# Optimization experiments

Hardware: AMD Instinct MI355X
Metric: run time of the kernel (lower is better)

Reference implementation:

```python
import jax, jax.numpy as jnp
import numpy as np

B = 32768   # batch
D = 64      # latent_dimension_half
H = 256     # inner_dimension
T = D * (D + 1) // 2  # 2080 triangular outputs


def setup_inputs() -> dict:
    key = jax.random.key(0)
    ks = jax.random.split(key, 7)
    s = 0.05
    return {
        "x": jax.random.normal(ks[0], (B, D), dtype=jnp.float32),
        "W1": jax.random.normal(ks[1], (D, H), dtype=jnp.float32) * s,
        "b1": jax.random.normal(ks[2], (H,), dtype=jnp.float32) * s,
        "W2": jax.random.normal(ks[3], (H, H), dtype=jnp.float32) * s,
        "b2": jax.random.normal(ks[4], (H,), dtype=jnp.float32) * s,
        "W3": jax.random.normal(ks[5], (H, T), dtype=jnp.float32) * s,
        "b3": jax.random.normal(ks[6], (T,), dtype=jnp.float32) * s,
    }


def reference(x, W1, b1, W2, b2, W3, b3):
    d = x.shape[-1]  # latent_dimension_half
    h = jnp.tanh(x @ W1 + b1)
    h = jnp.tanh(h @ W2 + b2)
    t = jnp.tanh(h @ W3 + b3)  # [B, d*(d+1)/2]
    # scatter: first d entries -> diagonal (diagflat), rest -> strict upper
    # triangle in row-major order (matches torch boolean-mask assignment)
    di = np.arange(d)
    iu, ju = np.triu_indices(d, k=1)
    rows = np.concatenate([di, iu])
    cols = np.concatenate([di, ju])
    u = jnp.zeros((x.shape[0], d, d), dtype=t.dtype).at[:, rows, cols].set(t)
    # y[b] = u[b].T @ u[b]
    return jnp.einsum('bki,bkj->bij', u, u)
```

## Files before the change

kernel.cpp:

```cpp
#include <hip/hip_runtime.h>


typedef __bf16 bf16_t;
typedef bf16_t bf16x8 __attribute__((ext_vector_type(8)));
typedef float  f32x4  __attribute__((ext_vector_type(4)));

#define MFMA16(a, b, c) __builtin_amdgcn_mfma_f32_16x16x32_bf16((a), (b), (c), 0, 0, 0)

constexpr int SLOT  = 4608;
constexpr int ARENA = 73728;
constexpr int H2OFF = 147456;
constexpr int CTRL  = 155648;

__device__ __forceinline__ float fast_tanh(float x) {
  float cx = fminf(fmaxf(x, -30.0f), 30.0f);
  float t  = __expf(2.0f * cx);
  return (t - 1.0f) * __builtin_amdgcn_rcpf(t + 1.0f);
}

__device__ __forceinline__ bf16x8 zsel(bf16x8 f, bool keep) {
  union { bf16x8 v; unsigned int u[4]; } x;
  x.v = f;
  unsigned m = keep ? 0xFFFFFFFFu : 0u;
#pragma unroll
  for (int p = 0; p < 4; ++p) x.u[p] &= m;
  return x.v;
}

__device__ __forceinline__ void decode_p(int p, int& j, int& k) {
  int cc = p >> 3, e = p & 7;
  int b = 0;
  while (b < 7 && cc >= 4 * (b + 1) * (b + 2)) ++b;
  int rl  = b + 1;
  int rem = cc - 4 * b * (b + 1);
  j = 8 * b + rem / rl;
  k = (rem % rl) * 8 + e;
}

__device__ __forceinline__ void lds_arrive(unsigned* p, int lane) {
  asm volatile("s_waitcnt lgkmcnt(0)" ::: "memory");
  if (lane == 0) atomicAdd(p, 1u);
}
__device__ __forceinline__ void lds_wait(volatile unsigned* p, unsigned tgt) {
  while (*p < tgt) __builtin_amdgcn_s_sleep(2);
  asm volatile("" ::: "memory");
  __builtin_amdgcn_sched_barrier(0);
}

__global__ void prep_kernel(const float* __restrict__ W1, const float* __restrict__ W2,
                            const float* __restrict__ W3, const float* __restrict__ b3,
                            char* __restrict__ wsb) {
  int tid = blockIdx.x * 512 + threadIdx.x;
  bf16_t* ws = (bf16_t*)wsb;
  if (tid < 16384) {
    int n = tid >> 6, k = tid & 63;
    ws[tid] = (bf16_t)W1[k * 256 + n];
  } else if (tid < 81920) {
    int m = tid - 16384;
    int n = m >> 8, k = m & 255;
    ws[tid] = (bf16_t)W2[k * 256 + n];
  } else if (tid < 671744) {
    int m = tid - 81920;
    int t  = m >> 12;
    int r  = m & 4095;
    int kk = r >> 9;
    int g  = (r >> 7) & 3;
    int c  = (r >> 3) & 15;
    int e  = r & 7;
    int p  = t * 16 + c;
    int k  = kk * 32 + g * 8 + e;
    int j, kd;
    decode_p(p, j, kd);
    float v = 0.f;
    if (kd <= j) {
      int n_ref = (kd == j) ? j : (64 + kd * 63 - (kd * (kd - 1)) / 2 + j - kd - 1);
      v = W3[k * 2080 + n_ref];
    }
    ws[tid] = (bf16_t)v;
  } else if (tid < 674048) {
    int p = tid - 671744;
    int j, kd;
    decode_p(p, j, kd);
    float v = 0.f;
    if (kd <= j) {
      int n_ref = (kd == j) ? j : (64 + kd * 63 - (kd * (kd - 1)) / 2 + j - kd - 1);
      v = b3[n_ref];
    }
    ((float*)(wsb + 1343488))[p] = v;
  }
}

__device__ __forceinline__ void gram_store(char* slot, int sw, float* yb,
                                           int g, int c, int lane) {
  bf16x8 f0, f1, f2, f3, f2b, f3b;
#pragma unroll
  for (int ti = 0; ti < 4; ++ti) {
    int j = ti * 16 + c;
    int Q = j >> 3, s = j & 7;
    int ro = 16 * (4 * Q * (Q + 1) + s * (Q + 1));
    bf16x8 fa = *(const bf16x8*)(slot + ((ro + g * 16) ^ sw));
    if (ti == 0) f0 = zsel(fa, g * 8 <= j);
    if (ti == 1) f1 = zsel(fa, g * 8 <= j);
    if (ti == 2) f2 = fa;
    if (ti == 3) f3 = fa;
    if (ti >= 2) {
      bf16x8 fb = *(const bf16x8*)(slot + ((ro + 64 + g * 16) ^ sw));
      fb = zsel(fb, 32 + g * 8 <= j);
      if (ti == 2) f2b = fb;
      else         f3b = fb;
    }
  }

  bf16x8 fA[4] = {f0, f1, f2, f3};
  f32x4 acc[4][4];
#pragma unroll
  for (int ti = 0; ti < 4; ++ti)
#pragma unroll
    for (int tj = 0; tj < 4; ++tj) {
      f32x4 z = {0.f, 0.f, 0.f, 0.f};
      acc[ti][tj] = MFMA16(fA[ti], fA[tj], z);
    }
  acc[2][2] = MFMA16(f2b, f2b, acc[2][2]);
  acc[2][3] = MFMA16(f2b, f3b, acc[2][3]);
  acc[3][2] = MFMA16(f3b, f2b, acc[3][2]);
  acc[3][3] = MFMA16(f3b, f3b, acc[3][3]);

#pragma unroll
  for (int ti = 0; ti < 4; ++ti) {
#pragma unroll
    for (int tj = 0; tj < 4; ++tj)
#pragma unroll
      for (int r = 0; r < 4; ++r)
        *(float*)(slot + (g * 4 + r) * 256 + (tj * 16 + c) * 4) = acc[ti][tj][r];
#pragma unroll
    for (int ii = 0; ii < 4; ++ii) {
      f32x4 v = *(const f32x4*)(slot + ii * 1024 + lane * 16);
      __builtin_nontemporal_store(v, (f32x4*)(yb + ti * 1024 + ii * 256 + lane * 4));
    }
  }
}

__global__ void __launch_bounds__(768, 3)
hm_kernel(const float* __restrict__ x, const float* __restrict__ b1,
          const float* __restrict__ b2, const char* __restrict__ wsb,
          float* __restrict__ out) {
  extern __shared__ char smem[];
  const int tid  = threadIdx.x;
  const int w    = tid >> 6;
  const int lane = tid & 63;
  const int g    = lane >> 4;
  const int c    = lane & 15;
  const int blk  = blockIdx.x;

  const bf16_t* W1t = (const bf16_t*)wsb;
  const bf16_t* W2t = W1t + 16384;
  const bf16_t* W3q = W1t + 81920;
  const float*  b3p = (const float*)(wsb + 1343488);
  char* h2s = smem + H2OFF;
  unsigned* ctrl = (unsigned*)(smem + CTRL);

  if (tid < 40) ctrl[tid] = 0;
  __syncthreads();

  if (w < 8) {
    float bias1[2], bias2[2];
#pragma unroll
    for (int ni = 0; ni < 2; ++ni) {
      int n = (w * 2 + ni) * 16 + c;
      bias1[ni] = b1[n];
      bias2[ni] = b2[n];
    }

#pragma unroll 1
    for (int r = 0; r < 8; ++r) {
      char* cur = smem + (r & 1) * ARENA;
      char* xs  = cur;
      char* h1s = cur + 4096;

      if (r >= 2) lds_wait(&ctrl[32 + (r - 2)], 4);

      if (tid < 256) {
        f32x4 v = *(const f32x4*)(x + ((size_t)blk * 128 + r * 16) * 64 + tid * 4);
        int row = tid >> 4, col = (tid & 15) * 4;
        union { bf16_t b[4]; unsigned long long u; } pk;
        pk.b[0] = (bf16_t)v[0]; pk.b[1] = (bf16_t)v[1];
        pk.b[2] = (bf16_t)v[2]; pk.b[3] = (bf16_t)v[3];
        *(unsigned long long*)(xs + ((row * 128 + col * 2) ^ ((row & 7) << 4))) = pk.u;
      }
      lds_arrive(&ctrl[r * 3 + 0], lane); lds_wait(&ctrl[r * 3 + 0], 8);

      {
        bf16x8 a0 = *(const bf16x8*)(xs + ((c * 128 + g * 16) ^ ((c & 7) << 4)));
        bf16x8 a1 = *(const bf16x8*)(xs + ((c * 128 + 64 + g * 16) ^ ((c & 7) << 4)));
#pragma unroll
        for (int ni = 0; ni < 2; ++ni) {
          int n = (w * 2 + ni) * 16 + c;
          bf16x8 bw0 = *(const bf16x8*)(W1t + n * 64 + g * 8);
          bf16x8 bw1 = *(const bf16x8*)(W1t + n * 64 + 32 + g * 8);
          f32x4 acc = {0.f, 0.f, 0.f, 0.f};
          acc = MFMA16(a0, bw0, acc);
          acc = MFMA16(a1, bw1, acc);
#pragma unroll
          for (int rr = 0; rr < 4; ++rr) {
            int row = g * 4 + rr;
            float v = fast_tanh(acc[rr] + bias1[ni]);
            *(bf16_t*)(h1s + ((row * 512 + n * 2) ^ ((row & 7) << 4))) = (bf16_t)v;
          }
        }
      }
      lds_arrive(&ctrl[r * 3 + 1], lane); lds_wait(&ctrl[r * 3 + 1], 8);

#pragma unroll
      for (int ni = 0; ni < 2; ++ni) {
        int n = (w * 2 + ni) * 16 + c;
        f32x4 acc0 = {0.f, 0.f, 0.f, 0.f}, acc1 = {0.f, 0.f, 0.f, 0.f};
#pragma unroll
        for (int kk = 0; kk < 8; kk += 2) {
          bf16x8 a0 = *(const bf16x8*)(h1s + ((c * 512 + kk * 64 + g * 16) ^ ((c & 7) << 4)));
          bf16x8 a1 = *(const bf16x8*)(h1s + ((c * 512 + (kk + 1) * 64 + g * 16) ^ ((c & 7) << 4)));
          bf16x8 bw0 = *(const bf16x8*)(W2t + n * 256 + kk * 32 + g * 8);
          bf16x8 bw1 = *(const bf16x8*)(W2t + n * 256 + (kk + 1) * 32 + g * 8);
          acc0 = MFMA16(a0, bw0, acc0);
          acc1 = MFMA16(a1, bw1, acc1);
        }
        f32x4 acc = acc0 + acc1;
#pragma unroll
        for (int rr = 0; rr < 4; ++rr) {
          int row = g * 4 + rr;
          float v = fast_tanh(acc[rr] + bias2[ni]);
          *(bf16_t*)(h2s + ((row * 512 + n * 2) ^ ((row & 7) << 4))) = (bf16_t)v;
        }
      }
      lds_arrive(&ctrl[r * 3 + 2], lane); lds_wait(&ctrl[r * 3 + 2], 8);

      {
        bf16x8 a0 = *(const bf16x8*)(h2s + ((c * 512 + 0 * 64 + g * 16) ^ ((c & 7) << 4)));
        bf16x8 a1 = *(const bf16x8*)(h2s + ((c * 512 + 1 * 64 + g * 16) ^ ((c & 7) << 4)));
        bf16x8 a2 = *(const bf16x8*)(h2s + ((c * 512 + 2 * 64 + g * 16) ^ ((c & 7) << 4)));
        bf16x8 a3 = *(const bf16x8*)(h2s + ((c * 512 + 3 * 64 + g * 16) ^ ((c & 7) << 4)));
        bf16x8 a4 = *(const bf16x8*)(h2s + ((c * 512 + 4 * 64 + g * 16) ^ ((c & 7) << 4)));
        bf16x8 a5 = *(const bf16x8*)(h2s + ((c * 512 + 5 * 64 + g * 16) ^ ((c & 7) << 4)));
        bf16x8 a6 = *(const bf16x8*)(h2s + ((c * 512 + 6 * 64 + g * 16) ^ ((c & 7) << 4)));
        bf16x8 a7 = *(const bf16x8*)(h2s + ((c * 512 + 7 * 64 + g * 16) ^ ((c & 7) << 4)));

        char* tw = cur + (g * 4) * SLOT;
        const int swz = (g & 7) << 4;

        bf16x8 A0, A1, A2, A3, A4, A5, A6, A7; float Ab;
        bf16x8 B0, B1, B2, B3, B4, B5, B6, B7; float Bb;

#define ISSUE_T(S, TI)                                                              \
  do {                                                                              \
    int t_ = w + (TI) * 8;                                                          \
    const bf16_t* np_ = W3q + t_ * 4096 + lane * 8;                                 \
    asm volatile("global_load_dwordx4 %0, %1, off" : "=v"(S##0) : "v"(np_));            \
    asm volatile("global_load_dwordx4 %0, %1, off" : "=v"(S##1) : "v"(np_ + 512));      \
    asm volatile("global_load_dwordx4 %0, %1, off" : "=v"(S##2) : "v"(np_ + 1024));     \
    asm volatile("global_load_dwordx4 %0, %1, off" : "=v"(S##3) : "v"(np_ + 1536));     \
    asm volatile("global_load_dwordx4 %0, %1, off" : "=v"(S##4) : "v"(np_ + 2048));     \
    asm volatile("global_load_dwordx4 %0, %1, off" : "=v"(S##5) : "v"(np_ + 2560));     \
    asm volatile("global_load_dwordx4 %0, %1, off" : "=v"(S##6) : "v"(np_ + 3072));     \
    asm volatile("global_load_dwordx4 %0, %1, off" : "=v"(S##7) : "v"(np_ + 3584));     \
    asm volatile("global_load_dword %0, %1, off"   : "=v"(S##b) : "v"(b3p + t_ * 16 + c)); \
  } while (0)

#define WAIT_N(N)                                          \
  do {                                                     \
    asm volatile("s_waitcnt vmcnt(" #N ")" ::: "memory");  \
    __builtin_amdgcn_sched_barrier(0);                     \
  } while (0)

#define COMP_T(S, TI)                                                    \
  do {                                                                   \
    f32x4 acc0 = {S##b, S##b, S##b, S##b};                               \
    f32x4 acc1 = {0.f, 0.f, 0.f, 0.f};                                   \
    acc0 = MFMA16(a0, S##0, acc0); acc1 = MFMA16(a1, S##1, acc1);        \
    acc0 = MFMA16(a2, S##2, acc0); acc1 = MFMA16(a3, S##3, acc1);        \
    acc0 = MFMA16(a4, S##4, acc0); acc1 = MFMA16(a5, S##5, acc1);        \
    acc0 = MFMA16(a6, S##6, acc0); acc1 = MFMA16(a7, S##7, acc1);        \
    f32x4 accs = acc0 + acc1;                                            \
    int p_ = (w + (TI) * 8) * 16 + c;                                    \
    _Pragma("unroll")                                                    \
    for (int r_ = 0; r_ < 4; ++r_) {                                     \
      float v_ = fast_tanh(accs[r_]);                                    \
      *(bf16_t*)(tw + r_ * SLOT + ((p_ * 2) ^ swz)) = (bf16_t)v_;        \
    }                                                                    \
  } while (0)

        ISSUE_T(A, 0);
#pragma unroll 1
        for (int pr = 0; pr < 8; ++pr) {
          ISSUE_T(B, 2 * pr + 1);
          WAIT_N(9);
          COMP_T(A, 2 * pr);
          ISSUE_T(A, 2 * pr + 2);
          WAIT_N(9);
          COMP_T(B, 2 * pr + 1);
        }
        ISSUE_T(B, 17);
        WAIT_N(9);
        COMP_T(A, 16);
        WAIT_N(0);
        COMP_T(B, 17);

#undef ISSUE_T
#undef WAIT_N
#undef COMP_T
      }
      lds_arrive(&ctrl[24 + r], lane);
    }
  } else {
    int ww = w - 8;
#pragma unroll 1
    for (int r = 0; r < 8; ++r) {
      lds_wait(&ctrl[24 + r], 8);
      char* arena = smem + (r & 1) * ARENA;
#pragma unroll 1
      for (int bi = 0; bi < 4; ++bi) {
        int m = ww * 4 + bi;
        gram_store(arena + m * SLOT, ((m >> 2) & 7) << 4,
                   out + ((size_t)blk * 128 + r * 16 + m) * 4096,
                   g, c, lane);
      }
      lds_arrive(&ctrl[32 + r], lane);
    }
  }
}

extern "C" void kernel_launch(void* const* d_in, const int* in_sizes, int n_in,
                              void* d_out, int out_size, void* d_ws, size_t ws_size,
                              hipStream_t stream) {
  (void)in_sizes; (void)n_in; (void)out_size; (void)ws_size;
  const float* x  = (const float*)d_in[0];
  const float* W1 = (const float*)d_in[1];
  const float* b1 = (const float*)d_in[2];
  const float* W2 = (const float*)d_in[3];
  const float* b2 = (const float*)d_in[4];
  const float* W3 = (const float*)d_in[5];
  const float* b3 = (const float*)d_in[6];
  char* wsb = (char*)d_ws;
  float* out = (float*)d_out;

  prep_kernel<<<1317, 512, 0, stream>>>(W1, W2, W3, b3, wsb);

  hipFuncSetAttribute((const void*)hm_kernel,
                      hipFuncAttributeMaxDynamicSharedMemorySize, 155904);
  hm_kernel<<<256, 768, 155904, stream>>>(x, b1, b2, wsb, out);
}
```

Before: 191.1 us.

## Process 32 rows per round so each W3 fragment load feeds two row-tiles

The layer-3 pass now handles two 16-row halves per round, so each loaded W3 fragment is used for two MFMA chains. This halves the W3 global traffic per block and the number of rounds. To make room, the double-buffered arenas are replaced by one 32-slot arena plus a shared scratch region, with a single reusable phase-barrier counter. x is now loaded straight into registers instead of staged through LDS. In exchange, register pressure rises (16 activation fragments held live), and the producer waves can no longer overlap with the gram-store waves across rounds, because they must wait for the single arena to drain.

```diff
diff --git a/kernel.cpp b/kernel.cpp
--- a/kernel.cpp
+++ b/kernel.cpp
@@ -8,8 +8,7 @@
 #define MFMA16(a, b, c) __builtin_amdgcn_mfma_f32_16x16x32_bf16((a), (b), (c), 0, 0, 0)
 
 constexpr int SLOT  = 4608;
-constexpr int ARENA = 73728;
-constexpr int H2OFF = 147456;
+constexpr int REG8  = 147456;
 constexpr int CTRL  = 155648;
 
 __device__ __forceinline__ float fast_tanh(float x) {
@@ -37,11 +36,11 @@
   k = (rem % rl) * 8 + e;
 }
 
-__device__ __forceinline__ void lds_arrive(unsigned* p, int lane) {
+__device__ __forceinline__ void ctr_arrive(unsigned* p, int lane) {
   asm volatile("s_waitcnt lgkmcnt(0)" ::: "memory");
   if (lane == 0) atomicAdd(p, 1u);
 }
-__device__ __forceinline__ void lds_wait(volatile unsigned* p, unsigned tgt) {
+__device__ __forceinline__ void ctr_wait(volatile unsigned* p, unsigned tgt) {
   while (*p < tgt) __builtin_amdgcn_s_sleep(2);
   asm volatile("" ::: "memory");
   __builtin_amdgcn_sched_barrier(0);
@@ -110,7 +109,6 @@
       else         f3b = fb;
     }
   }
-
   bf16x8 fA[4] = {f0, f1, f2, f3};
   f32x4 acc[4][4];
 #pragma unroll
@@ -124,7 +122,6 @@
   acc[2][3] = MFMA16(f2b, f3b, acc[2][3]);
   acc[3][2] = MFMA16(f3b, f2b, acc[3][2]);
   acc[3][3] = MFMA16(f3b, f3b, acc[3][3]);
-
 #pragma unroll
   for (int ti = 0; ti < 4; ++ti) {
 #pragma unroll
@@ -156,10 +153,10 @@
   const bf16_t* W2t = W1t + 16384;
   const bf16_t* W3q = W1t + 81920;
   const float*  b3p = (const float*)(wsb + 1343488);
-  char* h2s = smem + H2OFF;
+  char* reg8 = smem + REG8;
   unsigned* ctrl = (unsigned*)(smem + CTRL);
 
-  if (tid < 40) ctrl[tid] = 0;
+  if (tid < 3) ctrl[tid] = 0;
   __syncthreads();
 
   if (w < 8) {
@@ -170,28 +167,25 @@
       bias1[ni] = b1[n];
       bias2[ni] = b2[n];
     }
+    unsigned pb = 0;
+#define PBAR() do { ++pb; ctr_arrive(&ctrl[0], lane); ctr_wait(&ctrl[0], 8u * pb); } while (0)
 
 #pragma unroll 1
-    for (int r = 0; r < 8; ++r) {
-      char* cur = smem + (r & 1) * ARENA;
-      char* xs  = cur;
-      char* h1s = cur + 4096;
-
-      if (r >= 2) lds_wait(&ctrl[32 + (r - 2)], 4);
-
-      if (tid < 256) {
-        f32x4 v = *(const f32x4*)(x + ((size_t)blk * 128 + r * 16) * 64 + tid * 4);
-        int row = tid >> 4, col = (tid & 15) * 4;
-        union { bf16_t b[4]; unsigned long long u; } pk;
-        pk.b[0] = (bf16_t)v[0]; pk.b[1] = (bf16_t)v[1];
-        pk.b[2] = (bf16_t)v[2]; pk.b[3] = (bf16_t)v[3];
-        *(unsigned long long*)(xs + ((row * 128 + col * 2) ^ ((row & 7) << 4))) = pk.u;
-      }
-      lds_arrive(&ctrl[r * 3 + 0], lane); lds_wait(&ctrl[r * 3 + 0], 8);
-
-      {
-        bf16x8 a0 = *(const bf16x8*)(xs + ((c * 128 + g * 16) ^ ((c & 7) << 4)));
-        bf16x8 a1 = *(const bf16x8*)(xs + ((c * 128 + 64 + g * 16) ^ ((c & 7) << 4)));
+    for (int r = 0; r < 4; ++r) {
+      bf16x8 aF[2][8];
+#pragma unroll
+      for (int h = 0; h < 2; ++h) {
+        const float* xr = x + ((size_t)blk * 128 + r * 32 + h * 16 + c) * 64;
+        f32x4 u0 = *(const f32x4*)(xr + g * 8);
+        f32x4 u1 = *(const f32x4*)(xr + g * 8 + 4);
+        f32x4 v0 = *(const f32x4*)(xr + 32 + g * 8);
+        f32x4 v1 = *(const f32x4*)(xr + 32 + g * 8 + 4);
+        bf16x8 a0, a1;
+#pragma unroll
+        for (int i = 0; i < 4; ++i) {
+          a0[i] = (bf16_t)u0[i]; a0[4 + i] = (bf16_t)u1[i];
+          a1[i] = (bf16_t)v0[i]; a1[4 + i] = (bf16_t)v1[i];
+        }
 #pragma unroll
         for (int ni = 0; ni < 2; ++ni) {
           int n = (w * 2 + ni) * 16 + c;
@@ -204,47 +198,51 @@
           for (int rr = 0; rr < 4; ++rr) {
             int row = g * 4 + rr;
             float v = fast_tanh(acc[rr] + bias1[ni]);
-            *(bf16_t*)(h1s + ((row * 512 + n * 2) ^ ((row & 7) << 4))) = (bf16_t)v;
+            *(bf16_t*)(reg8 + ((row * 512 + n * 2) ^ ((row & 7) << 4))) = (bf16_t)v;
           }
         }
+        PBAR();
+        f32x4 h2a[2];
+#pragma unroll
+        for (int ni = 0; ni < 2; ++ni) {
+          int n = (w * 2 + ni) * 16 + c;
+          f32x4 acc0 = {0.f, 0.f, 0.f, 0.f}, acc1 = {0.f, 0.f, 0.f, 0.f};
+#pragma unroll
+          for (int kk = 0; kk < 8; kk += 2) {
+            bf16x8 p0 = *(const bf16x8*)(reg8 + ((c * 512 + kk * 64 + g * 16) ^ ((c & 7) << 4)));
+            bf16x8 p1 = *(const bf16x8*)(reg8 + ((c * 512 + (kk + 1) * 64 + g * 16) ^ ((c & 7) << 4)));
+            bf16x8 bw0 = *(const bf16x8*)(W2t + n * 256 + kk * 32 + g * 8);
+            bf16x8 bw1 = *(const bf16x8*)(W2t + n * 256 + (kk + 1) * 32 + g * 8);
+            acc0 = MFMA16(p0, bw0, acc0);
+            acc1 = MFMA16(p1, bw1, acc1);
+          }
+          h2a[ni] = acc0 + acc1;
+        }
+        PBAR();
+#pragma unroll
+        for (int ni = 0; ni < 2; ++ni) {
+          int n = (w * 2 + ni) * 16 + c;
+#pragma unroll
+          for (int rr = 0; rr < 4; ++rr) {
+            int row = g * 4 + rr;
+            float v = fast_tanh(h2a[ni][rr] + bias2[ni]);
+            *(bf16_t*)(reg8 + ((row * 512 + n * 2) ^ ((row & 7) << 4))) = (bf16_t)v;
+          }
+        }
+        PBAR();
+#pragma unroll
+        for (int k = 0; k < 8; ++k)
+          aF[h][k] = *(const bf16x8*)(reg8 + ((c * 512 + k * 64 + g * 16) ^ ((c & 7) << 4)));
+        PBAR();
       }
-      lds_arrive(&ctrl[r * 3 + 1], lane); lds_wait(&ctrl[r * 3 + 1], 8);
-
-#pragma unroll
-      for (int ni = 0; ni < 2; ++ni) {
-        int n = (w * 2 + ni) * 16 + c;
-        f32x4 acc0 = {0.f, 0.f, 0.f, 0.f}, acc1 = {0.f, 0.f, 0.f, 0.f};
-#pragma unroll
-        for (int kk = 0; kk < 8; kk += 2) {
-          bf16x8 a0 = *(const bf16x8*)(h1s + ((c * 512 + kk * 64 + g * 16) ^ ((c & 7) << 4)));
-          bf16x8 a1 = *(const bf16x8*)(h1s + ((c * 512 + (kk + 1) * 64 + g * 16) ^ ((c & 7) << 4)));
-          bf16x8 bw0 = *(const bf16x8*)(W2t + n * 256 + kk * 32 + g * 8);
-          bf16x8 bw1 = *(const bf16x8*)(W2t + n * 256 + (kk + 1) * 32 + g * 8);
-          acc0 = MFMA16(a0, bw0, acc0);
-          acc1 = MFMA16(a1, bw1, acc1);
-        }
-        f32x4 acc = acc0 + acc1;
-#pragma unroll
-        for (int rr = 0; rr < 4; ++rr) {
-          int row = g * 4 + rr;
-          float v = fast_tanh(acc[rr] + bias2[ni]);
-          *(bf16_t*)(h2s + ((row * 512 + n * 2) ^ ((row & 7) << 4))) = (bf16_t)v;
-        }
-      }
-      lds_arrive(&ctrl[r * 3 + 2], lane); lds_wait(&ctrl[r * 3 + 2], 8);
+
+      if (r > 0) ctr_wait(&ctrl[2], 4u * r);
 
       {
-        bf16x8 a0 = *(const bf16x8*)(h2s + ((c * 512 + 0 * 64 + g * 16) ^ ((c & 7) << 4)));
-        bf16x8 a1 = *(const bf16x8*)(h2s + ((c * 512 + 1 * 64 + g * 16) ^ ((c & 7) << 4)));
-        bf16x8 a2 = *(const bf16x8*)(h2s + ((c * 512 + 2 * 64 + g * 16) ^ ((c & 7) << 4)));
-        bf16x8 a3 = *(const bf16x8*)(h2s + ((c * 512 + 3 * 64 + g * 16) ^ ((c & 7) << 4)));
-        bf16x8 a4 = *(const bf16x8*)(h2s + ((c * 512 + 4 * 64 + g * 16) ^ ((c & 7) << 4)));
-        bf16x8 a5 = *(const bf16x8*)(h2s + ((c * 512 + 5 * 64 + g * 16) ^ ((c & 7) << 4)));
-        bf16x8 a6 = *(const bf16x8*)(h2s + ((c * 512 + 6 * 64 + g * 16) ^ ((c & 7) << 4)));
-        bf16x8 a7 = *(const bf16x8*)(h2s + ((c * 512 + 7 * 64 + g * 16) ^ ((c & 7) << 4)));
-
-        char* tw = cur + (g * 4) * SLOT;
-        const int swz = (g & 7) << 4;
+        char* twL = smem + (g * 4) * SLOT;
+        char* twH = smem + (16 + g * 4) * SLOT;
+        const int swzL = (g & 7) << 4;
+        const int swzH = ((4 + g) & 7) << 4;
 
         bf16x8 A0, A1, A2, A3, A4, A5, A6, A7; float Ab;
         bf16x8 B0, B1, B2, B3, B4, B5, B6, B7; float Bb;
@@ -270,21 +268,28 @@
     __builtin_amdgcn_sched_barrier(0);                     \
   } while (0)
 
-#define COMP_T(S, TI)                                                    \
-  do {                                                                   \
-    f32x4 acc0 = {S##b, S##b, S##b, S##b};                               \
-    f32x4 acc1 = {0.f, 0.f, 0.f, 0.f};                                   \
-    acc0 = MFMA16(a0, S##0, acc0); acc1 = MFMA16(a1, S##1, acc1);        \
-    acc0 = MFMA16(a2, S##2, acc0); acc1 = MFMA16(a3, S##3, acc1);        \
-    acc0 = MFMA16(a4, S##4, acc0); acc1 = MFMA16(a5, S##5, acc1);        \
-    acc0 = MFMA16(a6, S##6, acc0); acc1 = MFMA16(a7, S##7, acc1);        \
-    f32x4 accs = acc0 + acc1;                                            \
-    int p_ = (w + (TI) * 8) * 16 + c;                                    \
-    _Pragma("unroll")                                                    \
-    for (int r_ = 0; r_ < 4; ++r_) {                                     \
-      float v_ = fast_tanh(accs[r_]);                                    \
-      *(bf16_t*)(tw + r_ * SLOT + ((p_ * 2) ^ swz)) = (bf16_t)v_;        \
-    }                                                                    \
+#define COMP_T(S, TI)                                                        \
+  do {                                                                       \
+    f32x4 al0 = {S##b, S##b, S##b, S##b}, al1 = {0.f, 0.f, 0.f, 0.f};        \
+    f32x4 ah0 = {S##b, S##b, S##b, S##b}, ah1 = {0.f, 0.f, 0.f, 0.f};        \
+    al0 = MFMA16(aF[0][0], S##0, al0); al1 = MFMA16(aF[0][1], S##1, al1);    \
+    ah0 = MFMA16(aF[1][0], S##0, ah0); ah1 = MFMA16(aF[1][1], S##1, ah1);    \
+    al0 = MFMA16(aF[0][2], S##2, al0); al1 = MFMA16(aF[0][3], S##3, al1);    \
+    ah0 = MFMA16(aF[1][2], S##2, ah0); ah1 = MFMA16(aF[1][3], S##3, ah1);    \
+    al0 = MFMA16(aF[0][4], S##4, al0); al1 = MFMA16(aF[0][5], S##5, al1);    \
+    ah0 = MFMA16(aF[1][4], S##4, ah0); ah1 = MFMA16(aF[1][5], S##5, ah1);    \
+    al0 = MFMA16(aF[0][6], S##6, al0); al1 = MFMA16(aF[0][7], S##7, al1);    \
+    ah0 = MFMA16(aF[1][6], S##6, ah0); ah1 = MFMA16(aF[1][7], S##7, ah1);    \
+    f32x4 asL = al0 + al1;                                                   \
+    f32x4 asH = ah0 + ah1;                                                   \
+    int p_ = (w + (TI) * 8) * 16 + c;                                        \
+    _Pragma("unroll")                                                        \
+    for (int r_ = 0; r_ < 4; ++r_) {                                         \
+      float vL = fast_tanh(asL[r_]);                                         \
+      *(bf16_t*)(twL + r_ * SLOT + ((p_ * 2) ^ swzL)) = (bf16_t)vL;          \
+      float vH = fast_tanh(asH[r_]);                                         \
+      *(bf16_t*)(twH + r_ * SLOT + ((p_ * 2) ^ swzH)) = (bf16_t)vH;          \
+    }                                                                        \
   } while (0)
 
         ISSUE_T(A, 0);
@@ -307,22 +312,22 @@
 #undef WAIT_N
 #undef COMP_T
       }
-      lds_arrive(&ctrl[24 + r], lane);
-    }
+      ctr_arrive(&ctrl[1], lane);
+    }
+#undef PBAR
   } else {
     int ww = w - 8;
 #pragma unroll 1
-    for (int r = 0; r < 8; ++r) {
-      lds_wait(&ctrl[24 + r], 8);
-      char* arena = smem + (r & 1) * ARENA;
+    for (int r = 0; r < 4; ++r) {
+      ctr_wait(&ctrl[1], 8u * (r + 1));
 #pragma unroll 1
-      for (int bi = 0; bi < 4; ++bi) {
-        int m = ww * 4 + bi;
-        gram_store(arena + m * SLOT, ((m >> 2) & 7) << 4,
-                   out + ((size_t)blk * 128 + r * 16 + m) * 4096,
+      for (int bi = 0; bi < 8; ++bi) {
+        int m = ww * 8 + bi;
+        gram_store(smem + m * SLOT, ((m >> 2) & 7) << 4,
+                   out + ((size_t)blk * 128 + r * 32 + m) * 4096,
                    g, c, lane);
       }
-      lds_arrive(&ctrl[32 + r], lane);
+      ctr_arrive(&ctrl[2], lane);
     }
   }
 }
@@ -344,6 +349,6 @@
   prep_kernel<<<1317, 512, 0, stream>>>(W1, W2, W3, b3, wsb);
 
   hipFuncSetAttribute((const void*)hm_kernel,
-                      hipFuncAttributeMaxDynamicSharedMemorySize, 155904);
-  hm_kernel<<<256, 768, 155904, stream>>>(x, b1, b2, wsb, out);
-}
+                      hipFuncAttributeMaxDynamicSharedMemorySize, 155664);
+  hm_kernel<<<256, 768, 155664, stream>>>(x, b1, b2, wsb, out);
+}
```

New measurement: 199.0 us. 4.1% more time.
